# Kernel optimization log

Hardware: AMD Instinct MI355X
Metric: run time of the kernel (lower is better)

## Reference

```python
import jax, jax.numpy as jnp
import numpy as np

PAST, FUT = 64, 16
SB = 2048
N = PAST + FUT  # 80
OUTP = 35       # sum(emb dims) + 3


def _pre(cat, num, emb0, emb1, emb2, W1, b1, W2, b2, W3, b3):
    # pre_processing: embeddings + last-3 numeric cols -> MLP -> concat target col
    e = jnp.concatenate([emb0[cat[:, 0]], emb1[cat[:, 1]], emb2[cat[:, 2]]], -1)
    o = jnp.concatenate([e, num], -1)                 # [n, 35]
    h = jax.nn.relu(o @ W1 + b1)
    h = jax.nn.relu(h @ W2 + b2)
    h = h @ W3 + b3                                   # [n, 34]
    return jnp.concatenate([h, num[:, -1:]], -1)      # [n, 35]


def _gcn(x, src, dst, W, b):
    n = x.shape[0]
    h = x @ W
    deg = 1.0 + jax.ops.segment_sum(jnp.ones(src.shape, x.dtype), dst, num_segments=n)
    dinv = jax.lax.rsqrt(deg)
    msg = h[src] * (dinv[src] * dinv[dst])[:, None]
    agg = jax.ops.segment_sum(msg, dst, num_segments=n) + h * (dinv * dinv)[:, None]
    return agg + b


def _forward(x1_cat, x1_num, x2_cat, x2_num, e1, e2,
             emb0, emb1, emb2, pW1, pb1, pW2, pb2, pW3, pb3,
             g1W1, g1b1, g1W2, g1b2, g2W1, g2b1, g2W2, g2b2,
             kerW, smoothing, M):
    # masked-softmax adjacency A = softmax(relu(M M^T) masked to lower-tri, axis=1)
    Araw = jax.nn.relu(M @ M.T)
    tril = jnp.tril(jnp.ones((N, N), Araw.dtype))
    A = jax.nn.softmax(jnp.where(tril == 0, -jnp.inf, Araw), axis=1)

    x = _pre(x1_cat, x1_num, emb0, emb1, emb2, pW1, pb1, pW2, pb2, pW3, pb3)   # [SB*PAST, 35]
    x2 = _pre(x2_cat, x2_num, emb0, emb1, emb2, pW1, pb1, pW2, pb2, pW3, pb3)
    x2 = x2.reshape(SB, FUT, OUTP)

    # gnn1: GCN(35->64) -> ReLU -> GCN(64->34)
    h = jax.nn.relu(_gcn(x, e1[0], e1[1], g1W1, g1b1))
    x1 = _gcn(h, e1[0], e1[1], g1W2, g1b2).reshape(SB, PAST, OUTP - 1)

    x_kernel = jnp.concatenate([x1, x2[:, :, :-1]], -2)        # [SB, N, 34]
    y_kernel = x.reshape(SB, PAST, OUTP)[:, :, -1:]            # [SB, PAST, 1]

    # Mahalanobis kernel attention
    theta = kerW @ kerW.T
    theta = (theta + theta.T) / 2
    x_p = x_kernel[:, :PAST, :]
    x_f = x_kernel[:, PAST:, :]
    diff = x_p[:, None, :, :] - x_f[:, :, None, :]             # [SB, FUT, PAST, 34]
    # diagonal of diff @ theta @ diff^T, computed directly
    alpha = jnp.einsum('bqpo,oO,bqpO->bqp', diff, theta, diff)
    alpha = -0.5 * alpha / (jax.nn.sigmoid(smoothing[0]) * 0.01)
    A_tmp = A[PAST:, :PAST]                                    # [FUT, PAST]
    alpha = jnp.where(A_tmp[None] == 0, -jnp.inf, alpha)
    alpha = jax.nn.softmax(alpha, -1)
    yh = jnp.einsum('bqp,bpo->bqo', alpha, y_kernel)           # [SB, FUT, 1]

    x2 = jnp.concatenate([x2[:, :, :-1], yh], -1)              # [SB, FUT, 35]
    # gnn2: GCN(35->64) -> ReLU -> GCN(64->1)
    h2 = jax.nn.relu(_gcn(x2.reshape(-1, OUTP), e2[0], e2[1], g2W1, g2b1))
    out = _gcn(h2, e2[0], e2[1], g2W2, g2b2).reshape(SB, FUT)

    # cdist over concatenated past+future features, via norm trick
    xa = jnp.concatenate([x.reshape(SB, PAST, OUTP), x2], -2)  # [SB, N, 35]
    sq = jnp.sum(xa * xa, -1)
    d2 = sq[:, :, None] + sq[:, None, :] - 2.0 * jnp.einsum('bnd,bmd->bnm', xa, xa)
    cd = jnp.sqrt(jnp.maximum(d2, 0.0))
    return out, cd, A


def setup_inputs():
    key = jax.random.key(0)
    ks = jax.random.split(key, 24)
    f32 = jnp.float32
    n1, n2 = SB * PAST, SB * FUT
    E1, E2 = n1 * 8, n2 * 8
    return {
        'x1_cat': jax.random.randint(ks[0], (n1, 3), 0, 7, dtype=jnp.int32),
        'x1_num': jax.random.normal(ks[1], (n1, 3), f32),
        'x2_cat': jax.random.randint(ks[2], (n2, 3), 0, 7, dtype=jnp.int32),
        'x2_num': jax.random.normal(ks[3], (n2, 3), f32),
        'edge_index1': jax.random.randint(ks[4], (2, E1), 0, n1, dtype=jnp.int32),
        'edge_index2': jax.random.randint(ks[5], (2, E2), 0, n2, dtype=jnp.int32),
        'emb0': jax.random.normal(ks[6], (24, 16), f32),
        'emb1': jax.random.normal(ks[7], (7, 8), f32),
        'emb2': jax.random.normal(ks[8], (12, 8), f32),
        'pre_W1': jax.random.normal(ks[9], (35, 128), f32) * 0.1,
        'pre_b1': jnp.zeros((128,), f32),
        'pre_W2': jax.random.normal(ks[10], (128, 128), f32) * 0.08,
        'pre_b2': jnp.zeros((128,), f32),
        'pre_W3': jax.random.normal(ks[11], (128, 34), f32) * 0.08,
        'pre_b3': jnp.zeros((34,), f32),
        'g1_W1': jax.random.normal(ks[12], (35, 64), f32) * 0.1,
        'g1_b1': jnp.zeros((64,), f32),
        'g1_W2': jax.random.normal(ks[13], (64, 34), f32) * 0.1,
        'g1_b2': jnp.zeros((34,), f32),
        'g2_W1': jax.random.normal(ks[14], (35, 64), f32) * 0.1,
        'g2_b1': jnp.zeros((64,), f32),
        'g2_W2': jax.random.normal(ks[15], (64, 1), f32) * 0.1,
        'g2_b2': jnp.zeros((1,), f32),
        'ker_W': jax.random.normal(ks[16], (34, 128), f32) * 0.1,
        'smoothing': jax.random.normal(ks[17], (1,), f32),
        'M': jax.random.normal(ks[18], (N, N // 3), f32) * 0.1,
    }


def reference(x1_cat, x1_num, x2_cat, x2_num, edge_index1, edge_index2,
              emb0, emb1, emb2, pre_W1, pre_b1, pre_W2, pre_b2, pre_W3, pre_b3,
              g1_W1, g1_b1, g1_W2, g1_b2, g2_W1, g2_b1, g2_W2, g2_b2,
              ker_W, smoothing, M):
    return _forward(x1_cat, x1_num, x2_cat, x2_num, edge_index1, edge_index2,
                    emb0, emb1, emb2, pre_W1, pre_b1, pre_W2, pre_b2, pre_W3, pre_b3,
                    g1_W1, g1_b1, g1_W2, g1_b2, g2_W1, g2_b1, g2_W2, g2_b2,
                    ker_W, smoothing, M)
```

## Files before the change

### kernel.cpp

```cpp
#include <hip/hip_runtime.h>
#include <math.h>

#define PASTN 64
#define FUTN 16
#define NN 80

__global__ __launch_bounds__(256) void k_setup(const float* __restrict__ M, const float* __restrict__ kerW,
                                               const float* __restrict__ smoothing,
                                               float* __restrict__ A_ws, float* __restrict__ A_out,
                                               float* __restrict__ theta, float* __restrict__ scale)
{
    __shared__ float Ms[80 * 26];
    __shared__ float Ar[80 * 80];
    const int t = threadIdx.x;
    for (int i = t; i < 80 * 26; i += 256) Ms[i] = M[i];
    __syncthreads();
    for (int idx = t; idx < 6400; idx += 256) {
        int i = idx / 80, j = idx - 80 * i;
        float acc = 0.f;
#pragma unroll
        for (int k = 0; k < 26; ++k) acc = fmaf(Ms[i * 26 + k], Ms[j * 26 + k], acc);
        Ar[idx] = fmaxf(acc, 0.f);
    }
    __syncthreads();
    if (t < 80) {
        float mx = -1e30f;
        for (int j = 0; j <= t; ++j) mx = fmaxf(mx, Ar[t * 80 + j]);
        float s = 0.f;
        for (int j = 0; j <= t; ++j) s += expf(Ar[t * 80 + j] - mx);
        float inv = 1.f / s;
        for (int j = 0; j < 80; ++j) {
            float v = (j <= t) ? expf(Ar[t * 80 + j] - mx) * inv : 0.f;
            A_ws[t * 80 + j] = v;
            A_out[t * 80 + j] = v;
        }
    }
    for (int idx = t; idx < 34 * 34; idx += 256) {
        int i = idx / 34, j = idx - 34 * i;
        float acc = 0.f;
        for (int k = 0; k < 128; ++k) acc = fmaf(kerW[i * 128 + k], kerW[j * 128 + k], acc);
        theta[idx] = acc;
    }
    if (t == 0) {
        float s0 = smoothing[0];
        float sig = 1.f / (1.f + expf(-s0));
        scale[0] = -0.5f / (sig * 0.01f);
    }
}

__global__ void k_deg2(const int* __restrict__ dst1, const int* __restrict__ dst2,
                       int* __restrict__ deg1, int* __restrict__ deg2,
                       int E1, int E2, int nbe1)
{
    int gb = blockIdx.x;
    if (gb < nbe1) {
        int e = gb * 256 + threadIdx.x;
        if (e < E1) atomicAdd(&deg1[dst1[e]], 1);
    } else {
        int e = (gb - nbe1) * 256 + threadIdx.x;
        if (e < E2) atomicAdd(&deg2[dst2[e]], 1);
    }
}

#define SCHUNK 1024
__global__ __launch_bounds__(256) void k_scan_reduce2(const int* __restrict__ deg1, const int* __restrict__ deg2,
                                                      int* __restrict__ bsumA, int* __restrict__ bsumB,
                                                      int n1, int n2, int nb1)
{
    __shared__ int sd[256];
    const int gb = blockIdx.x, t = threadIdx.x;
    const int which = (gb < nb1) ? 0 : 1;
    const int b = which ? gb - nb1 : gb;
    const int* deg = which ? deg2 : deg1;
    const int n = which ? n2 : n1;
    const int base = b * SCHUNK;
    int s = 0;
#pragma unroll
    for (int j = 0; j < 4; ++j) {
        int i = base + t + j * 256;
        if (i < n) s += deg[i];
    }
    sd[t] = s;
    __syncthreads();
    for (int o = 128; o > 0; o >>= 1) {
        if (t < o) sd[t] += sd[t + o];
        __syncthreads();
    }
    if (t == 0) (which ? bsumB : bsumA)[b] = sd[0];
}

__global__ __launch_bounds__(1024) void k_scan_mid2(int* __restrict__ bsumA, int* __restrict__ bsumB,
                                                    int nbA, int nbB)
{
    __shared__ int sd[1024];
    const int t = threadIdx.x;
    int* bsum = (blockIdx.x == 0) ? bsumA : bsumB;
    int nb = (blockIdx.x == 0) ? nbA : nbB;
    int orig = (t < nb) ? bsum[t] : 0;
    sd[t] = orig;
    __syncthreads();
    for (int o = 1; o < 1024; o <<= 1) {
        int v = (t >= o) ? sd[t - o] : 0;
        __syncthreads();
        sd[t] += v;
        __syncthreads();
    }
    if (t < nb) bsum[t] = sd[t] - orig;
}

__global__ __launch_bounds__(256) void k_scan_final2(const int* __restrict__ deg1, const int* __restrict__ deg2,
                                                     const int* __restrict__ bsumA, const int* __restrict__ bsumB,
                                                     int* __restrict__ rs1, int* __restrict__ rs2,
                                                     int* __restrict__ cur1, int* __restrict__ cur2,
                                                     float* __restrict__ dinv1, float* __restrict__ dinv2,
                                                     int n1, int n2, int nb1)
{
    __shared__ int sd[256];
    const int gb = blockIdx.x, t = threadIdx.x;
    const int which = (gb < nb1) ? 0 : 1;
    const int b = which ? gb - nb1 : gb;
    const int* deg = which ? deg2 : deg1;
    const int* bsum = which ? bsumB : bsumA;
    int* rs = which ? rs2 : rs1;
    int* cur = which ? cur2 : cur1;
    float* dinv = which ? dinv2 : dinv1;
    const int n = which ? n2 : n1;
    const int base = b * SCHUNK + t * 4;
    int v0 = (base + 0 < n) ? deg[base + 0] : 0;
    int v1 = (base + 1 < n) ? deg[base + 1] : 0;
    int v2 = (base + 2 < n) ? deg[base + 2] : 0;
    int v3 = (base + 3 < n) ? deg[base + 3] : 0;
    int tsum = v0 + v1 + v2 + v3;
    sd[t] = tsum;
    __syncthreads();
    int incl = tsum;
    for (int o = 1; o < 256; o <<= 1) {
        int v = (t >= o) ? sd[t - o] : 0;
        __syncthreads();
        incl += v;
        sd[t] = incl;
        __syncthreads();
    }
    int off = bsum[b] + incl - tsum;
    if (base + 0 < n) { rs[base + 0] = off;            cur[base + 0] = off;            dinv[base + 0] = rsqrtf(1.f + (float)v0); }
    if (base + 1 < n) { rs[base + 1] = off + v0;       cur[base + 1] = off + v0;       dinv[base + 1] = rsqrtf(1.f + (float)v1); }
    if (base + 2 < n) { rs[base + 2] = off + v0 + v1;  cur[base + 2] = off + v0 + v1;  dinv[base + 2] = rsqrtf(1.f + (float)v2); }
    if (base + 3 < n) { rs[base + 3] = off + v0 + v1 + v2; cur[base + 3] = off + v0 + v1 + v2; dinv[base + 3] = rsqrtf(1.f + (float)v3); }
}

__global__ void k_fill2(const int* __restrict__ src1, const int* __restrict__ dst1,
                        const int* __restrict__ src2, const int* __restrict__ dst2,
                        int* __restrict__ cur1, int* __restrict__ cur2,
                        int* __restrict__ out1, int* __restrict__ out2,
                        int E1, int E2, int nbe1)
{
    int gb = blockIdx.x;
    if (gb < nbe1) {
        int e = gb * 256 + threadIdx.x;
        if (e < E1) { int pos = atomicAdd(&cur1[dst1[e]], 1); out1[pos] = src1[e]; }
    } else {
        int e = (gb - nbe1) * 256 + threadIdx.x;
        if (e < E2) { int pos = atomicAdd(&cur2[dst2[e]], 1); out2[pos] = src2[e]; }
    }
}

template <int DIN>
__global__ __launch_bounds__(256) void k_gcn_s(const int* __restrict__ rs, const int* __restrict__ deg,
                                               const int* __restrict__ srcs, const float* __restrict__ dinv,
                                               const float* __restrict__ Hs, const float* __restrict__ W,
                                               const float* __restrict__ b, float* __restrict__ Out, int n)
{
    const int w = threadIdx.x >> 6, lane = threadIdx.x & 63;
    const int row = blockIdx.x * 4 + w;
    __shared__ float ag[4][DIN];
    const float di = dinv[row];
    const int e0 = rs[row];
    const int d = deg[row];
    float acc = (lane < DIN) ? Hs[(size_t)row * DIN + lane] : 0.f;
    int e = 0;
    for (; e + 8 <= d; e += 8) {
        int s0 = srcs[e0 + e + 0], s1 = srcs[e0 + e + 1], s2 = srcs[e0 + e + 2], s3 = srcs[e0 + e + 3];
        int s4 = srcs[e0 + e + 4], s5 = srcs[e0 + e + 5], s6 = srcs[e0 + e + 6], s7 = srcs[e0 + e + 7];
        float h0 = 0.f, h1 = 0.f, h2 = 0.f, h3 = 0.f, h4 = 0.f, h5 = 0.f, h6 = 0.f, h7 = 0.f;
        if (lane < DIN) {
            h0 = Hs[(size_t)s0 * DIN + lane]; h1 = Hs[(size_t)s1 * DIN + lane];
            h2 = Hs[(size_t)s2 * DIN + lane]; h3 = Hs[(size_t)s3 * DIN + lane];
            h4 = Hs[(size_t)s4 * DIN + lane]; h5 = Hs[(size_t)s5 * DIN + lane];
            h6 = Hs[(size_t)s6 * DIN + lane]; h7 = Hs[(size_t)s7 * DIN + lane];
        }
        acc += ((h0 + h1) + (h2 + h3)) + ((h4 + h5) + (h6 + h7));
    }
    for (; e + 4 <= d; e += 4) {
        int s0 = srcs[e0 + e + 0], s1 = srcs[e0 + e + 1], s2 = srcs[e0 + e + 2], s3 = srcs[e0 + e + 3];
        float h0 = 0.f, h1 = 0.f, h2 = 0.f, h3 = 0.f;
        if (lane < DIN) {
            h0 = Hs[(size_t)s0 * DIN + lane]; h1 = Hs[(size_t)s1 * DIN + lane];
            h2 = Hs[(size_t)s2 * DIN + lane]; h3 = Hs[(size_t)s3 * DIN + lane];
        }
        acc += (h0 + h1) + (h2 + h3);
    }
    for (; e < d; ++e) {
        int s = srcs[e0 + e];
        if (lane < DIN) acc += Hs[(size_t)s * DIN + lane];
    }
    if (lane < DIN) ag[w][lane] = acc;
    __syncthreads();
    float o = 0.f;
#pragma unroll
    for (int i = 0; i < DIN; ++i) o = fmaf(ag[w][i], W[i * 64 + lane], o);
    Out[(size_t)row * 64 + lane] = fmaxf(fmaf(di, o, b[lane]), 0.f);
}

template <int D>
__global__ __launch_bounds__(256) void k_pcomb_s(const int* __restrict__ rs, const int* __restrict__ deg,
                                                 const int* __restrict__ srcs, const float* __restrict__ dinv,
                                                 const float* __restrict__ Hs, const float* __restrict__ b,
                                                 float* __restrict__ dest, int n)
{
    const int wid = (blockIdx.x * blockDim.x + threadIdx.x) >> 6;
    const int lane = threadIdx.x & 63;
    if (wid >= n) return;
    const float di = dinv[wid];
    const int e0 = rs[wid];
    const int d = deg[wid];
    float acc = (lane < D) ? Hs[(size_t)wid * D + lane] : 0.f;
    int e = 0;
    for (; e + 8 <= d; e += 8) {
        int s0 = srcs[e0 + e + 0], s1 = srcs[e0 + e + 1], s2 = srcs[e0 + e + 2], s3 = srcs[e0 + e + 3];
        int s4 = srcs[e0 + e + 4], s5 = srcs[e0 + e + 5], s6 = srcs[e0 + e + 6], s7 = srcs[e0 + e + 7];
        float h0 = 0.f, h1 = 0.f, h2 = 0.f, h3 = 0.f, h4 = 0.f, h5 = 0.f, h6 = 0.f, h7 = 0.f;
        if (lane < D) {
            h0 = Hs[(size_t)s0 * D + lane]; h1 = Hs[(size_t)s1 * D + lane];
            h2 = Hs[(size_t)s2 * D + lane]; h3 = Hs[(size_t)s3 * D + lane];
            h4 = Hs[(size_t)s4 * D + lane]; h5 = Hs[(size_t)s5 * D + lane];
            h6 = Hs[(size_t)s6 * D + lane]; h7 = Hs[(size_t)s7 * D + lane];
        }
        acc += ((h0 + h1) + (h2 + h3)) + ((h4 + h5) + (h6 + h7));
    }
    for (; e + 4 <= d; e += 4) {
        int s0 = srcs[e0 + e + 0], s1 = srcs[e0 + e + 1], s2 = srcs[e0 + e + 2], s3 = srcs[e0 + e + 3];
        float h0 = 0.f, h1 = 0.f, h2 = 0.f, h3 = 0.f;
        if (lane < D) {
            h0 = Hs[(size_t)s0 * D + lane]; h1 = Hs[(size_t)s1 * D + lane];
            h2 = Hs[(size_t)s2 * D + lane]; h3 = Hs[(size_t)s3 * D + lane];
        }
        acc += (h0 + h1) + (h2 + h3);
    }
    for (; e < d; ++e) {
        int s = srcs[e0 + e];
        if (lane < D) acc += Hs[(size_t)s * D + lane];
    }
    if (lane < D) dest[(size_t)wid * D + lane] = fmaf(di, acc, b[lane]);
}

__global__ void k_pcomb1_s(const int* __restrict__ rs, const int* __restrict__ deg,
                           const int* __restrict__ srcs, const float* __restrict__ dinv,
                           const float* __restrict__ Hs, const float* __restrict__ b,
                           float* __restrict__ dest, int n)
{
    int r = blockIdx.x * blockDim.x + threadIdx.x;
    if (r >= n) return;
    int e0 = rs[r], d = deg[r];
    float acc = Hs[r];
    int e = 0;
    for (; e + 8 <= d; e += 8) {
        acc += ((Hs[srcs[e0 + e + 0]] + Hs[srcs[e0 + e + 1]]) + (Hs[srcs[e0 + e + 2]] + Hs[srcs[e0 + e + 3]]))
             + ((Hs[srcs[e0 + e + 4]] + Hs[srcs[e0 + e + 5]]) + (Hs[srcs[e0 + e + 6]] + Hs[srcs[e0 + e + 7]]));
    }
    for (; e + 4 <= d; e += 4) {
        acc += (Hs[srcs[e0 + e + 0]] + Hs[srcs[e0 + e + 1]]) + (Hs[srcs[e0 + e + 2]] + Hs[srcs[e0 + e + 3]]);
    }
    for (; e < d; ++e) acc += Hs[srcs[e0 + e]];
    dest[r] = fmaf(dinv[r], acc, b[0]);
}

#define PR 32
__global__ __launch_bounds__(256) void k_pre_all(const int* __restrict__ cat1, const float* __restrict__ num1,
                                                 const int* __restrict__ cat2, const float* __restrict__ num2,
                                                 const float* __restrict__ emb0, const float* __restrict__ emb1,
                                                 const float* __restrict__ emb2,
                                                 const float* __restrict__ W1, const float* __restrict__ b1,
                                                 const float* __restrict__ W2, const float* __restrict__ b2,
                                                 const float* __restrict__ W3, const float* __restrict__ b3,
                                                 const float* __restrict__ dinv1, const float* __restrict__ dinv2,
                                                 float* __restrict__ X1, float* __restrict__ Xs1,
                                                 float* __restrict__ X2, float* __restrict__ Xs2,
                                                 int nblk1)
{
    __shared__ float oT[35 * PR];
    __shared__ float h1T[128 * PR];
    __shared__ float h2T[128 * PR];
    const int t = threadIdx.x;
    const int ct = t & 31;
    const int rg = t >> 5;
    const int gb = blockIdx.x;
    const int g2 = (gb >= nblk1);
    const int* cat = g2 ? cat2 : cat1;
    const float* num = g2 ? num2 : num1;
    const float* dinv = g2 ? dinv2 : dinv1;
    float* X = g2 ? X2 : X1;
    float* Xs = g2 ? Xs2 : Xs1;
    const int base = (g2 ? gb - nblk1 : gb) * PR;

    for (int idx = t; idx < 35 * PR; idx += 256) {
        int i = idx >> 5, r = idx & 31;
        int row = base + r;
        float v;
        if (i < 16) v = emb0[cat[row * 3 + 0] * 16 + i];
        else if (i < 24) v = emb1[cat[row * 3 + 1] * 8 + (i - 16)];
        else if (i < 32) v = emb2[cat[row * 3 + 2] * 8 + (i - 24)];
        else v = num[row * 3 + (i - 32)];
        oT[i * PR + (((r >> 2) ^ (i & 7)) << 2) + (r & 3)] = v;
    }
    __syncthreads();

    float acc[4][4];
    {
        float4 bb = *(const float4*)(b1 + 4 * ct);
        const float bbv[4] = {bb.x, bb.y, bb.z, bb.w};
#pragma unroll
        for (int c = 0; c < 4; ++c)
#pragma unroll
            for (int r = 0; r < 4; ++r) acc[c][r] = bbv[c];
#pragma unroll
        for (int kk = 0; kk < 32; kk += 8) {
#pragma unroll
            for (int u = 0; u < 8; ++u) {
                const int i = kk + u;
                float4 ov = *(const float4*)(oT + i * PR + ((rg ^ u) << 2));
                float4 wv = *(const float4*)(W1 + i * 128 + 4 * ct);
                const float o4[4] = {ov.x, ov.y, ov.z, ov.w};
                const float w4[4] = {wv.x, wv.y, wv.z, wv.w};
#pragma unroll
                for (int c = 0; c < 4; ++c)
#pragma unroll
                    for (int r = 0; r < 4; ++r) acc[c][r] = fmaf(w4[c], o4[r], acc[c][r]);
            }
        }
#pragma unroll
        for (int u = 0; u < 3; ++u) {
            const int i = 32 + u;
            float4 ov = *(const float4*)(oT + i * PR + ((rg ^ u) << 2));
            float4 wv = *(const float4*)(W1 + i * 128 + 4 * ct);
            const float o4[4] = {ov.x, ov.y, ov.z, ov.w};
            const float w4[4] = {wv.x, wv.y, wv.z, wv.w};
#pragma unroll
            for (int c = 0; c < 4; ++c)
#pragma unroll
                for (int r = 0; r < 4; ++r) acc[c][r] = fmaf(w4[c], o4[r], acc[c][r]);
        }
#pragma unroll
        for (int j = 0; j < 4; ++j) {
            int c = (ct + j) & 3;
            int col = 4 * ct + c;
            float4 v;
            v.x = fmaxf(acc[c][0], 0.f);
            v.y = fmaxf(acc[c][1], 0.f);
            v.z = fmaxf(acc[c][2], 0.f);
            v.w = fmaxf(acc[c][3], 0.f);
            *(float4*)(h1T + col * PR + ((rg ^ (col & 7)) << 2)) = v;
        }
    }
    __syncthreads();
    {
        float4 bb = *(const float4*)(b2 + 4 * ct);
        const float bbv[4] = {bb.x, bb.y, bb.z, bb.w};
#pragma unroll
        for (int c = 0; c < 4; ++c)
#pragma unroll
            for (int r = 0; r < 4; ++r) acc[c][r] = bbv[c];
        for (int kk = 0; kk < 128; kk += 8) {
#pragma unroll
            for (int u = 0; u < 8; ++u) {
                const int k = kk + u;
                float4 hv = *(const float4*)(h1T + k * PR + ((rg ^ u) << 2));
                float4 wv = *(const float4*)(W2 + k * 128 + 4 * ct);
                const float h4[4] = {hv.x, hv.y, hv.z, hv.w};
                const float w4[4] = {wv.x, wv.y, wv.z, wv.w};
#pragma unroll
                for (int c = 0; c < 4; ++c)
#pragma unroll
                    for (int r = 0; r < 4; ++r) acc[c][r] = fmaf(w4[c], h4[r], acc[c][r]);
            }
        }
#pragma unroll
        for (int j = 0; j < 4; ++j) {
            int c = (ct + j) & 3;
            int col = 4 * ct + c;
            float4 v;
            v.x = fmaxf(acc[c][0], 0.f);
            v.y = fmaxf(acc[c][1], 0.f);
            v.z = fmaxf(acc[c][2], 0.f);
            v.w = fmaxf(acc[c][3], 0.f);
            *(float4*)(h2T + col * PR + ((rg ^ (col & 7)) << 2)) = v;
        }
    }
    __syncthreads();
    for (int task = t; task < 34 * 8; task += 256) {
        int j = task >> 3, rg3 = task & 7;
        float a0 = b3[j], a1 = a0, a2 = a0, a3 = a0;
        for (int kk = 0; kk < 128; kk += 8) {
#pragma unroll
            for (int u = 0; u < 8; ++u) {
                const int k = kk + u;
                float4 hv = *(const float4*)(h2T + k * PR + ((rg3 ^ u) << 2));
                float wv = W3[k * 34 + j];
                a0 = fmaf(hv.x, wv, a0);
                a1 = fmaf(hv.y, wv, a1);
                a2 = fmaf(hv.z, wv, a2);
                a3 = fmaf(hv.w, wv, a3);
            }
        }
        size_t rb = (size_t)(base + rg3 * 4);
        float d0 = dinv[rb + 0], d1 = dinv[rb + 1], d2 = dinv[rb + 2], d3 = dinv[rb + 3];
        X[(rb + 0) * 35 + j] = a0;  Xs[(rb + 0) * 35 + j] = a0 * d0;
        X[(rb + 1) * 35 + j] = a1;  Xs[(rb + 1) * 35 + j] = a1 * d1;
        X[(rb + 2) * 35 + j] = a2;  Xs[(rb + 2) * 35 + j] = a2 * d2;
        X[(rb + 3) * 35 + j] = a3;  Xs[(rb + 3) * 35 + j] = a3 * d3;
    }
    if (t < PR) {
        int row = base + t;
        float v = num[row * 3 + 2];
        X[(size_t)row * 35 + 34] = v;
        Xs[(size_t)row * 35 + 34] = v * dinv[row];
    }
}

template <int DIN, int DOUT, bool BIAS, bool RELU, bool SCALE>
__global__ void k_gemm(const float* __restrict__ Xin, int ldin, const float* __restrict__ W,
                       const float* __restrict__ b, const float* __restrict__ oscale,
                       float* __restrict__ Out, int n)
{
    __shared__ float Ws[DIN * DOUT];
    for (int i = threadIdx.x; i < DIN * DOUT; i += blockDim.x) Ws[i] = W[i];
    __syncthreads();
    int idx = blockIdx.x * blockDim.x + threadIdx.x;
    if (idx >= n * DOUT) return;
    int row = idx / DOUT, j = idx - row * DOUT;
    const float4* xr4 = (const float4*)(Xin + (size_t)row * ldin);
    float acc = BIAS ? b[j] : 0.f;
#pragma unroll
    for (int i4 = 0; i4 < DIN / 4; ++i4) {
        float4 x = xr4[i4];
        acc = fmaf(x.x, Ws[(4 * i4 + 0) * DOUT + j], acc);
        acc = fmaf(x.y, Ws[(4 * i4 + 1) * DOUT + j], acc);
        acc = fmaf(x.z, Ws[(4 * i4 + 2) * DOUT + j], acc);
        acc = fmaf(x.w, Ws[(4 * i4 + 3) * DOUT + j], acc);
    }
    if (RELU) acc = fmaxf(acc, 0.f);
    if (SCALE) acc *= oscale[row];
    Out[idx] = acc;
}

__global__ __launch_bounds__(256) void k_alpha(const float* __restrict__ X1,
                                               const float* __restrict__ X,
                                               float* __restrict__ X2,
                                               float* __restrict__ Xs2,
                                               const float* __restrict__ dinv2,
                                               const float* __restrict__ theta,
                                               const float* __restrict__ A,
                                               const float* __restrict__ scale)
{
    const int b = blockIdx.x;
    const int t = threadIdx.x;
    const int p = t & 63;
    const int w = t >> 6;
    __shared__ float th[34 * 34];
    __shared__ float xpS[64 * 35];
    __shared__ float xfS[16 * 34];
    __shared__ float UfS[16 * 34];
    __shared__ float upPart[4][64];
    __shared__ float upS[64];
    __shared__ float yS[64];

    for (int i = t; i < 34 * 34; i += 256) th[i] = theta[i];
    for (int i = t; i < 64 * 34; i += 256) {
        int r = i / 34, o = i - 34 * r;
        xpS[r * 35 + o] = X1[(size_t)(b * 64 + r) * 34 + o];
    }
    for (int i = t; i < 16 * 34; i += 256) {
        int q = i / 34, o = i - 34 * q;
        xfS[i] = X2[(size_t)(b * 16 + q) * 35 + o];
    }
    if (t < 64) yS[t] = X[(size_t)(b * 64 + t) * 35 + 34];
    __syncthreads();

    for (int i = t; i < 16 * 34; i += 256) {
        int q = i / 34, o = i - 34 * q;
        float a = 0.f;
#pragma unroll
        for (int O = 0; O < 34; ++O) a = fmaf(th[o * 34 + O], xfS[q * 34 + O], a);
        UfS[i] = a;
    }
    {
        const int o0 = w * 9;
        const int o1 = (o0 + 9 < 34) ? o0 + 9 : 34;
        float a = 0.f;
        for (int o = o0; o < o1; ++o) {
            float s2 = 0.f;
#pragma unroll
            for (int O = 0; O < 34; ++O) s2 = fmaf(th[o * 34 + O], xpS[p * 35 + O], s2);
            a = fmaf(xpS[p * 35 + o], s2, a);
        }
        upPart[w][p] = a;
    }
    __syncthreads();
    if (t < 64) upS[t] = upPart[0][t] + upPart[1][t] + upPart[2][t] + upPart[3][t];
    __syncthreads();

    const float sc = scale[0];
    const float up = upS[p];
    const float y = yS[p];
#pragma unroll
    for (int i = 0; i < 4; ++i) {
        const int q = w + 4 * i;
        float g = 0.f;
#pragma unroll
        for (int o = 0; o < 34; ++o) g = fmaf(UfS[q * 34 + o], xpS[p * 35 + o], g);
        float a = sc * (up - 2.f * g);
        if (A[(PASTN + q) * NN + p] == 0.f) a = -INFINITY;
        float mx = a;
#pragma unroll
        for (int off = 32; off > 0; off >>= 1) mx = fmaxf(mx, __shfl_xor(mx, off));
        float e = expf(a - mx);
        float s = e;
#pragma unroll
        for (int off = 32; off > 0; off >>= 1) s += __shfl_xor(s, off);
        float c = (e / s) * y;
#pragma unroll
        for (int off = 32; off > 0; off >>= 1) c += __shfl_xor(c, off);
        if (p == 0) {
            size_t ridx = (size_t)(b * 16 + q);
            X2[ridx * 35 + 34] = c;
            Xs2[ridx * 35 + 34] = c * dinv2[ridx];
        }
    }
}

__global__ __launch_bounds__(256) void k_cd(const float* __restrict__ X, const float* __restrict__ X2,
                                            float* __restrict__ cd)
{
    const int b = blockIdx.x;
    const int t = threadIdx.x;
    __shared__ float xa[80 * 44];
    __shared__ float sq[80];
    for (int idx = t; idx < 80 * 44; idx += 256) {
        int nrow = idx / 44, k = idx - 44 * nrow;
        float v = 0.f;
        if (k < 35)
            v = (nrow < 64) ? X[(size_t)(b * 64 + nrow) * 35 + k]
                            : X2[(size_t)(b * 16 + (nrow - 64)) * 35 + k];
        xa[idx] = v;
    }
    __syncthreads();
    const float4* xa4 = (const float4*)xa;
    if (t < 80) {
        float acc = 0.f;
#pragma unroll
        for (int c = 0; c < 9; ++c) {
            float4 v = xa4[t * 11 + c];
            acc = fmaf(v.x, v.x, fmaf(v.y, v.y, fmaf(v.z, v.z, fmaf(v.w, v.w, acc))));
        }
        sq[t] = acc;
    }
    __syncthreads();
    const int ti = t >> 4;
    const int tj = t & 15;
    float dot[5][5];
#pragma unroll
    for (int r = 0; r < 5; ++r)
#pragma unroll
        for (int c = 0; c < 5; ++c) dot[r][c] = 0.f;
#pragma unroll
    for (int ch = 0; ch < 9; ++ch) {
        float4 av[5], bv[5];
#pragma unroll
        for (int r = 0; r < 5; ++r) av[r] = xa4[(5 * ti + r) * 11 + ch];
#pragma unroll
        for (int c = 0; c < 5; ++c) bv[c] = xa4[(5 * tj + c) * 11 + ch];
#pragma unroll
        for (int r = 0; r < 5; ++r)
#pragma unroll
            for (int c = 0; c < 5; ++c)
                dot[r][c] = fmaf(av[r].x, bv[c].x, fmaf(av[r].y, bv[c].y,
                              fmaf(av[r].z, bv[c].z, fmaf(av[r].w, bv[c].w, dot[r][c]))));
    }
    float* out = cd + (size_t)b * 6400;
#pragma unroll
    for (int r = 0; r < 5; ++r) {
        int n_ = 5 * ti + r;
        float sn = sq[n_];
#pragma unroll
        for (int c = 0; c < 5; ++c) {
            int m = 5 * tj + c;
            float d2 = sn + sq[m] - 2.f * dot[r][c];
            out[n_ * 80 + m] = sqrtf(fmaxf(d2, 0.f));
        }
    }
}

extern "C" void kernel_launch(void* const* d_in, const int* in_sizes, int n_in,
                              void* d_out, int out_size, void* d_ws, size_t ws_size,
                              hipStream_t stream)
{
    const int* x1_cat = (const int*)d_in[0];
    const float* x1_num = (const float*)d_in[1];
    const int* x2_cat = (const int*)d_in[2];
    const float* x2_num = (const float*)d_in[3];
    const int* e1 = (const int*)d_in[4];
    const int* e2 = (const int*)d_in[5];
    const float* emb0 = (const float*)d_in[6];
    const float* emb1 = (const float*)d_in[7];
    const float* emb2 = (const float*)d_in[8];
    const float* pW1 = (const float*)d_in[9];
    const float* pb1 = (const float*)d_in[10];
    const float* pW2 = (const float*)d_in[11];
    const float* pb2 = (const float*)d_in[12];
    const float* pW3 = (const float*)d_in[13];
    const float* pb3 = (const float*)d_in[14];
    const float* g1W1 = (const float*)d_in[15];
    const float* g1b1 = (const float*)d_in[16];
    const float* g1W2 = (const float*)d_in[17];
    const float* g1b2 = (const float*)d_in[18];
    const float* g2W1 = (const float*)d_in[19];
    const float* g2b1 = (const float*)d_in[20];
    const float* g2W2 = (const float*)d_in[21];
    const float* g2b2 = (const float*)d_in[22];
    const float* kerW = (const float*)d_in[23];
    const float* smoothing = (const float*)d_in[24];
    const float* M = (const float*)d_in[25];

    const int n1 = in_sizes[0] / 3;
    const int n2 = in_sizes[2] / 3;
    const int E1 = in_sizes[4] / 2;
    const int E2 = in_sizes[5] / 2;
    const int SBc = n2 / FUTN;

    float* w = (float*)d_ws;
    size_t off = 0;
    float* scale = w + off; off += 16;
    float* theta = w + off; off += 1184;
    float* Aws = w + off; off += 6400;
    float* X = w + off; off += (size_t)n1 * 35;
    float* Xs1 = w + off; off += (size_t)n1 * 35;
    float* X2 = w + off; off += (size_t)n2 * 35;
    float* Xs2 = w + off; off += (size_t)n2 * 35;
    float* dinv1 = w + off; off += (size_t)n1;
    float* dinv2 = w + off; off += (size_t)n2;
    float* B2 = w + off; off += (size_t)n1 * 64;
    float* B3 = w + off; off += (size_t)n1 * 34;
    float* B4 = w + off; off += (size_t)n1 * 34;
    int* iw = (int*)(w + off);
    size_t ioff = 0;
    int* degi1 = iw + ioff; ioff += n1;
    int* degi2 = iw + ioff; ioff += n2;
    int* rs1 = iw + ioff; ioff += n1;
    int* cur1 = iw + ioff; ioff += n1;
    int* srcs1 = iw + ioff; ioff += E1;
    int* rs2 = iw + ioff; ioff += n2;
    int* cur2 = iw + ioff; ioff += n2;
    int* srcs2 = iw + ioff; ioff += E2;
    int* bsumA = iw + ioff; ioff += 1024;
    int* bsumB = iw + ioff; ioff += 1024;

    float* out_f = (float*)d_out;
    float* cd_f = out_f + (size_t)SBc * FUTN;
    float* A_out = cd_f + (size_t)SBc * NN * NN;

    auto cdiv = [](long long a, long long b) { return (unsigned)((a + b - 1) / b); };

    hipMemsetAsync(degi1, 0, ((size_t)n1 + n2) * 4, stream);
    k_setup<<<1, 256, 0, stream>>>(M, kerW, smoothing, Aws, A_out, theta, scale);

    const int nbe1 = cdiv(E1, 256), nbe2 = cdiv(E2, 256);
    k_deg2<<<nbe1 + nbe2, 256, 0, stream>>>(e1 + E1, e2 + E2, degi1, degi2, E1, E2, nbe1);

    const int nb1 = cdiv(n1, SCHUNK), nb2 = cdiv(n2, SCHUNK);
    k_scan_reduce2<<<nb1 + nb2, 256, 0, stream>>>(degi1, degi2, bsumA, bsumB, n1, n2, nb1);
    k_scan_mid2<<<2, 1024, 0, stream>>>(bsumA, bsumB, nb1, nb2);
    k_scan_final2<<<nb1 + nb2, 256, 0, stream>>>(degi1, degi2, bsumA, bsumB, rs1, rs2, cur1, cur2,
                                                 dinv1, dinv2, n1, n2, nb1);
    k_fill2<<<nbe1 + nbe2, 256, 0, stream>>>(e1, e1 + E1, e2, e2 + E2, cur1, cur2, srcs1, srcs2, E1, E2, nbe1);

    k_pre_all<<<n1 / PR + n2 / PR, 256, 0, stream>>>(x1_cat, x1_num, x2_cat, x2_num,
                                                     emb0, emb1, emb2, pW1, pb1, pW2, pb2, pW3, pb3,
                                                     dinv1, dinv2, X, Xs1, X2, Xs2, n1 / PR);

    k_gcn_s<35><<<cdiv(n1, 4), 256, 0, stream>>>(rs1, degi1, srcs1, dinv1, Xs1, g1W1, g1b1, B2, n1);

    k_gemm<64, 34, false, false, true><<<cdiv((long long)n1 * 34, 256), 256, 0, stream>>>(B2, 64, g1W2, nullptr, dinv1, B3, n1);
    k_pcomb_s<34><<<cdiv(n1, 4), 256, 0, stream>>>(rs1, degi1, srcs1, dinv1, B3, g1b2, B4, n1);

    k_alpha<<<SBc, 256, 0, stream>>>(B4, X, X2, Xs2, dinv2, theta, Aws, scale);

    k_gcn_s<35><<<cdiv(n2, 4), 256, 0, stream>>>(rs2, degi2, srcs2, dinv2, Xs2, g2W1, g2b1, B2, n2);

    k_gemm<64, 1, false, false, true><<<cdiv(n2, 256), 256, 0, stream>>>(B2, 64, g2W2, nullptr, dinv2, B3, n2);
    k_pcomb1_s<<<cdiv(n2, 256), 256, 0, stream>>>(rs2, degi2, srcs2, dinv2, B3, g2b2, out_f, n2);

    k_cd<<<SBc, 256, 0, stream>>>(X, X2, cd_f);
}
```

Measured before the change: 781.5 us.

## Run pre-MLP second layer on bf16x3 split MFMA instead of FP32 FMA

Splits the second 128x128 pre-processing MLP layer into bf16 hi/lo pairs and computes it with 16x16x32 bf16 MFMA instructions, using three products to approximate FP32 accuracy. A new small kernel pre-converts W2 into the MFMA fragment layout once per call, and the first layer now writes h1 as swizzled row-major bf16 hi/lo in LDS. LDS use shrinks because the oT and h2T buffers are aliased. The aim is to move the dominant FP32 FMA work onto matrix cores, at the cost of a small precision loss and an extra kernel launch.

```diff
diff --git a/kernel.cpp b/kernel.cpp
--- a/kernel.cpp
+++ b/kernel.cpp
@@ -4,6 +4,17 @@
 #define PASTN 64
 #define FUTN 16
 #define NN 80
+
+typedef __attribute__((ext_vector_type(8))) short sh8;
+typedef __attribute__((ext_vector_type(4))) float f32x4;
+
+__device__ __forceinline__ unsigned short f2bf(float f) {
+    unsigned int u = __float_as_uint(f);
+    return (unsigned short)((u + 0x7FFFu + ((u >> 16) & 1u)) >> 16);
+}
+__device__ __forceinline__ float bf2f(unsigned short s) {
+    return __uint_as_float(((unsigned int)s) << 16);
+}
 
 __global__ __launch_bounds__(256) void k_setup(const float* __restrict__ M, const float* __restrict__ kerW,
                                                const float* __restrict__ smoothing,
@@ -46,6 +57,19 @@
         float sig = 1.f / (1.f + expf(-s0));
         scale[0] = -0.5f / (sig * 0.01f);
     }
+}
+
+__global__ void k_wconv(const float* __restrict__ W2, unsigned short* __restrict__ Wh,
+                        unsigned short* __restrict__ Wl)
+{
+    int g = blockIdx.x * 256 + threadIdx.x;
+    int i = g & 7, ln = (g >> 3) & 63, ks = (g >> 9) & 3, nt = g >> 11;
+    int col = nt * 16 + (ln & 15);
+    int k = ks * 32 + ((ln >> 4) << 3) + i;
+    float w = W2[k * 128 + col];
+    unsigned short hi = f2bf(w);
+    Wh[g] = hi;
+    Wl[g] = f2bf(w - bf2f(hi));
 }
 
 __global__ void k_deg2(const int* __restrict__ dst1, const int* __restrict__ dst2,
@@ -280,16 +304,20 @@
                                                  const float* __restrict__ emb0, const float* __restrict__ emb1,
                                                  const float* __restrict__ emb2,
                                                  const float* __restrict__ W1, const float* __restrict__ b1,
-                                                 const float* __restrict__ W2, const float* __restrict__ b2,
+                                                 const unsigned short* __restrict__ W2fh,
+                                                 const unsigned short* __restrict__ W2fl,
+                                                 const float* __restrict__ b2,
                                                  const float* __restrict__ W3, const float* __restrict__ b3,
                                                  const float* __restrict__ dinv1, const float* __restrict__ dinv2,
                                                  float* __restrict__ X1, float* __restrict__ Xs1,
                                                  float* __restrict__ X2, float* __restrict__ Xs2,
                                                  int nblk1)
 {
-    __shared__ float oT[35 * PR];
-    __shared__ float h1T[128 * PR];
-    __shared__ float h2T[128 * PR];
+    __shared__ float ldsB[128 * 32];
+    __shared__ __align__(16) unsigned short h1h[128 * 32];
+    __shared__ __align__(16) unsigned short h1l[128 * 32];
+    float* oT = ldsB;
+    float* h2T = ldsB;
     const int t = threadIdx.x;
     const int ct = t & 31;
     const int rg = t >> 5;
@@ -314,33 +342,16 @@
     }
     __syncthreads();
 
-    float acc[4][4];
     {
+        float acc[4][4];
         float4 bb = *(const float4*)(b1 + 4 * ct);
         const float bbv[4] = {bb.x, bb.y, bb.z, bb.w};
 #pragma unroll
         for (int c = 0; c < 4; ++c)
 #pragma unroll
             for (int r = 0; r < 4; ++r) acc[c][r] = bbv[c];
-#pragma unroll
-        for (int kk = 0; kk < 32; kk += 8) {
-#pragma unroll
-            for (int u = 0; u < 8; ++u) {
-                const int i = kk + u;
-                float4 ov = *(const float4*)(oT + i * PR + ((rg ^ u) << 2));
-                float4 wv = *(const float4*)(W1 + i * 128 + 4 * ct);
-                const float o4[4] = {ov.x, ov.y, ov.z, ov.w};
-                const float w4[4] = {wv.x, wv.y, wv.z, wv.w};
-#pragma unroll
-                for (int c = 0; c < 4; ++c)
-#pragma unroll
-                    for (int r = 0; r < 4; ++r) acc[c][r] = fmaf(w4[c], o4[r], acc[c][r]);
-            }
-        }
-#pragma unroll
-        for (int u = 0; u < 3; ++u) {
-            const int i = 32 + u;
-            float4 ov = *(const float4*)(oT + i * PR + ((rg ^ u) << 2));
+        for (int i = 0; i < 35; ++i) {
+            float4 ov = *(const float4*)(oT + i * PR + ((rg ^ (i & 7)) << 2));
             float4 wv = *(const float4*)(W1 + i * 128 + 4 * ct);
             const float o4[4] = {ov.x, ov.y, ov.z, ov.w};
             const float w4[4] = {wv.x, wv.y, wv.z, wv.w};
@@ -351,65 +362,74 @@
         }
 #pragma unroll
         for (int j = 0; j < 4; ++j) {
-            int c = (ct + j) & 3;
-            int col = 4 * ct + c;
+            int row32 = 4 * rg + j;
+            int rowm = row32 & 15;
+            int off = row32 * 128 + ((((ct >> 1) ^ rowm)) << 3) + ((ct & 1) << 2);
+            ushort4 hi4, lo4;
+            float h0 = fmaxf(acc[0][j], 0.f);
+            float h1v = fmaxf(acc[1][j], 0.f);
+            float h2v = fmaxf(acc[2][j], 0.f);
+            float h3v = fmaxf(acc[3][j], 0.f);
+            hi4.x = f2bf(h0); lo4.x = f2bf(h0 - bf2f(hi4.x));
+            hi4.y = f2bf(h1v); lo4.y = f2bf(h1v - bf2f(hi4.y));
+            hi4.z = f2bf(h2v); lo4.z = f2bf(h2v - bf2f(hi4.z));
+            hi4.w = f2bf(h3v); lo4.w = f2bf(h3v - bf2f(hi4.w));
+            *(ushort4*)(h1h + off) = hi4;
+            *(ushort4*)(h1l + off) = lo4;
+        }
+    }
+    __syncthreads();
+
+    {
+        const int wv = t >> 6, ln = t & 63;
+        const int mt = wv & 1, ng = wv >> 1;
+        const int lr = ln & 15, lh = ln >> 4;
+        f32x4 acc[4];
+#pragma unroll
+        for (int j = 0; j < 4; ++j) acc[j] = (f32x4){0.f, 0.f, 0.f, 0.f};
+        const int arow = (mt * 16 + lr) * 128;
+#pragma unroll
+        for (int ks = 0; ks < 4; ++ks) {
+            const int sc = (((ks * 4 + lh) ^ lr) << 3);
+            sh8 ahi = *(const sh8*)(h1h + arow + sc);
+            sh8 alo = *(const sh8*)(h1l + arow + sc);
+#pragma unroll
+            for (int j = 0; j < 4; ++j) {
+                const int fbase = ((((ng * 4 + j) * 4 + ks) * 64 + ln) << 3);
+                sh8 bhi = *(const sh8*)(W2fh + fbase);
+                sh8 blo = *(const sh8*)(W2fl + fbase);
+                acc[j] = __builtin_amdgcn_mfma_f32_16x16x32_bf16(ahi, bhi, acc[j], 0, 0, 0);
+                acc[j] = __builtin_amdgcn_mfma_f32_16x16x32_bf16(ahi, blo, acc[j], 0, 0, 0);
+                acc[j] = __builtin_amdgcn_mfma_f32_16x16x32_bf16(alo, bhi, acc[j], 0, 0, 0);
+            }
+        }
+        __syncthreads();
+#pragma unroll
+        for (int j = 0; j < 4; ++j) {
+            int col = (ng * 4 + j) * 16 + lr;
+            int rg3 = mt * 4 + lh;
+            float bc = b2[col];
             float4 v;
-            v.x = fmaxf(acc[c][0], 0.f);
-            v.y = fmaxf(acc[c][1], 0.f);
-            v.z = fmaxf(acc[c][2], 0.f);
-            v.w = fmaxf(acc[c][3], 0.f);
-            *(float4*)(h1T + col * PR + ((rg ^ (col & 7)) << 2)) = v;
-        }
-    }
-    __syncthreads();
-    {
-        float4 bb = *(const float4*)(b2 + 4 * ct);
-        const float bbv[4] = {bb.x, bb.y, bb.z, bb.w};
-#pragma unroll
-        for (int c = 0; c < 4; ++c)
-#pragma unroll
-            for (int r = 0; r < 4; ++r) acc[c][r] = bbv[c];
-        for (int kk = 0; kk < 128; kk += 8) {
-#pragma unroll
-            for (int u = 0; u < 8; ++u) {
-                const int k = kk + u;
-                float4 hv = *(const float4*)(h1T + k * PR + ((rg ^ u) << 2));
-                float4 wv = *(const float4*)(W2 + k * 128 + 4 * ct);
-                const float h4[4] = {hv.x, hv.y, hv.z, hv.w};
-                const float w4[4] = {wv.x, wv.y, wv.z, wv.w};
-#pragma unroll
-                for (int c = 0; c < 4; ++c)
-#pragma unroll
-                    for (int r = 0; r < 4; ++r) acc[c][r] = fmaf(w4[c], h4[r], acc[c][r]);
-            }
-        }
-#pragma unroll
-        for (int j = 0; j < 4; ++j) {
-            int c = (ct + j) & 3;
-            int col = 4 * ct + c;
-            float4 v;
-            v.x = fmaxf(acc[c][0], 0.f);
-            v.y = fmaxf(acc[c][1], 0.f);
-            v.z = fmaxf(acc[c][2], 0.f);
-            v.w = fmaxf(acc[c][3], 0.f);
-            *(float4*)(h2T + col * PR + ((rg ^ (col & 7)) << 2)) = v;
-        }
-    }
-    __syncthreads();
+            v.x = fmaxf(acc[j][0] + bc, 0.f);
+            v.y = fmaxf(acc[j][1] + bc, 0.f);
+            v.z = fmaxf(acc[j][2] + bc, 0.f);
+            v.w = fmaxf(acc[j][3] + bc, 0.f);
+            *(float4*)(h2T + col * PR + ((rg3 ^ (col & 7)) << 2)) = v;
+        }
+    }
+    __syncthreads();
+
     for (int task = t; task < 34 * 8; task += 256) {
         int j = task >> 3, rg3 = task & 7;
         float a0 = b3[j], a1 = a0, a2 = a0, a3 = a0;
-        for (int kk = 0; kk < 128; kk += 8) {
-#pragma unroll
-            for (int u = 0; u < 8; ++u) {
-                const int k = kk + u;
-                float4 hv = *(const float4*)(h2T + k * PR + ((rg3 ^ u) << 2));
-                float wv = W3[k * 34 + j];
-                a0 = fmaf(hv.x, wv, a0);
-                a1 = fmaf(hv.y, wv, a1);
-                a2 = fmaf(hv.z, wv, a2);
-                a3 = fmaf(hv.w, wv, a3);
-            }
+#pragma unroll 4
+        for (int k = 0; k < 128; ++k) {
+            float4 hv = *(const float4*)(h2T + k * PR + ((rg3 ^ (k & 7)) << 2));
+            float wv = W3[k * 34 + j];
+            a0 = fmaf(hv.x, wv, a0);
+            a1 = fmaf(hv.y, wv, a1);
+            a2 = fmaf(hv.z, wv, a2);
+            a3 = fmaf(hv.w, wv, a3);
         }
         size_t rb = (size_t)(base + rg3 * 4);
         float d0 = dinv[rb + 0], d1 = dinv[rb + 1], d2 = dinv[rb + 2], d3 = dinv[rb + 3];
@@ -650,6 +670,9 @@
     float* B2 = w + off; off += (size_t)n1 * 64;
     float* B3 = w + off; off += (size_t)n1 * 34;
     float* B4 = w + off; off += (size_t)n1 * 34;
+    off = (off + 3) & ~(size_t)3;
+    unsigned short* W2fh = (unsigned short*)(w + off); off += 8192;
+    unsigned short* W2fl = (unsigned short*)(w + off); off += 8192;
     int* iw = (int*)(w + off);
     size_t ioff = 0;
     int* degi1 = iw + ioff; ioff += n1;
@@ -671,6 +694,7 @@
 
     hipMemsetAsync(degi1, 0, ((size_t)n1 + n2) * 4, stream);
     k_setup<<<1, 256, 0, stream>>>(M, kerW, smoothing, Aws, A_out, theta, scale);
+    k_wconv<<<64, 256, 0, stream>>>(pW2, W2fh, W2fl);
 
     const int nbe1 = cdiv(E1, 256), nbe2 = cdiv(E2, 256);
     k_deg2<<<nbe1 + nbe2, 256, 0, stream>>>(e1 + E1, e2 + E2, degi1, degi2, E1, E2, nbe1);
@@ -683,7 +707,7 @@
     k_fill2<<<nbe1 + nbe2, 256, 0, stream>>>(e1, e1 + E1, e2, e2 + E2, cur1, cur2, srcs1, srcs2, E1, E2, nbe1);
 
     k_pre_all<<<n1 / PR + n2 / PR, 256, 0, stream>>>(x1_cat, x1_num, x2_cat, x2_num,
-                                                     emb0, emb1, emb2, pW1, pb1, pW2, pb2, pW3, pb3,
+                                                     emb0, emb1, emb2, pW1, pb1, W2fh, W2fl, pb2, pW3, pb3,
                                                      dinv1, dinv2, X, Xs1, X2, Xs2, n1 / PR);
 
     k_gcn_s<35><<<cdiv(n1, 4), 256, 0, stream>>>(rs1, degi1, srcs1, dinv1, Xs1, g1W1, g1b1, B2, n1);
```

Result: faster. 710.0 us (-9.1%).
